# Performance work log

Hardware: AMD Instinct MI355X
Metric: run time of the kernel (lower is better)

Reference implementation:

```python
import jax, jax.numpy as jnp
import numpy as np

N, IN_DIM, OUT_DIM = 8192, 128, 128

def setup_inputs() -> dict:
    key = jax.random.key(0)
    k1, k2, k3, k4 = jax.random.split(key, 4)
    X = jax.random.normal(k1, (N, IN_DIM), dtype=jnp.float32)
    A = jax.random.uniform(k2, (N, N), dtype=jnp.float32)
    # nn.Linear(in_dim, out_dim): W [out,in], b [out]
    bound = 1.0 / np.sqrt(IN_DIM)
    W = jax.random.uniform(k3, (OUT_DIM, IN_DIM), minval=-bound, maxval=bound, dtype=jnp.float32)
    b = jax.random.uniform(k4, (OUT_DIM,), minval=-bound, maxval=bound, dtype=jnp.float32)
    return {"X": X, "A": A, "W": W, "b": b}

def reference(X, A, W, b):
    n = A.shape[0]
    A_hat = A + jnp.eye(n, dtype=A.dtype)                 # A + I
    d_inv_sqrt = A_hat.sum(axis=1) ** -0.5                # [N]
    # D^-1/2 @ A_hat @ D^-1/2 == row/col scaling (same math, no diag GEMMs)
    A_norm = d_inv_sqrt[:, None] * A_hat * d_inv_sqrt[None, :]
    H = A_norm @ X                                        # [N, in_dim]
    return H @ W.T + b                                    # [N, out_dim]
```

## Files before the change

kernel.cpp:

```cpp
#include <hip/hip_runtime.h>

#define N_NODES 8192
#define DIM 128

typedef short bf16x8 __attribute__((ext_vector_type(8)));
typedef unsigned short u16x4 __attribute__((ext_vector_type(4)));
typedef float f32x4 __attribute__((ext_vector_type(4)));

__device__ __forceinline__ unsigned short f2bf_rne(float x) {
    unsigned int u = __builtin_bit_cast(unsigned int, x);
    u += 0x7fffu + ((u >> 16) & 1u);
    return (unsigned short)(u >> 16);
}
__device__ __forceinline__ float bf2f(unsigned short h) {
    unsigned int u = ((unsigned int)h) << 16;
    return __builtin_bit_cast(float, u);
}

__global__ __launch_bounds__(256) void k_prep(const float* __restrict__ A,
                                              unsigned short* __restrict__ Abp,
                                              float* __restrict__ d) {
    __shared__ unsigned short tile[16 * 512];
    __shared__ float rs[2][8][128];
    const int t = threadIdx.x;
    const int lane = t & 63, wv = t >> 6;
    const int l15 = lane & 15, quad = lane >> 4;
    const int rb16 = blockIdx.x;
    const float* Ag0 = A + (size_t)rb16 * 16 * N_NODES;
    const int h = t >> 7;
    const int c4 = (t & 127) << 2;
    float rsum[8] = {};

    f32x4 pre[8];
#pragma unroll
    for (int i = 0; i < 8; ++i)
        pre[i] = *(const f32x4*)(Ag0 + (size_t)(h + 2 * i) * N_NODES + c4);

    for (int chunk = 0; chunk < 16; ++chunk) {
        f32x4 curv[8];
#pragma unroll
        for (int i = 0; i < 8; ++i) curv[i] = pre[i];
        if (chunk < 15) {
            const float* Ag = Ag0 + (chunk + 1) * 512;
#pragma unroll
            for (int i = 0; i < 8; ++i)
                pre[i] = *(const f32x4*)(Ag + (size_t)(h + 2 * i) * N_NODES + c4);
        }
        __syncthreads();
#pragma unroll
        for (int i = 0; i < 8; ++i) {
            int r = h + 2 * i;
            f32x4 v = curv[i];
            rsum[i] += (v[0] + v[1]) + (v[2] + v[3]);
            int byte = (r * 1024 + c4 * 2) ^ ((r & 7) << 4);
            u16x4 pk = { f2bf_rne(v[0]), f2bf_rne(v[1]), f2bf_rne(v[2]), f2bf_rne(v[3]) };
            *(u16x4*)((char*)tile + byte) = pk;
        }
        __syncthreads();
#pragma unroll
        for (int u = 0; u < 4; ++u) {
            int kk = wv * 4 + u;
            int abyte = (l15 * 1024 + (kk * 32 + quad * 8) * 2) ^ ((l15 & 7) << 4);
            bf16x8 frag = *(const bf16x8*)((const char*)tile + abyte);
            int kbg = chunk * 16 + kk;
            *(bf16x8*)(Abp + ((size_t)(rb16 * 256 + kbg) * 64 + lane) * 8) = frag;
        }
    }

#pragma unroll
    for (int i = 0; i < 8; ++i) rs[h][i][t & 127] = rsum[i];
    __syncthreads();
    if (t < 16) {
        const float* p = rs[t & 1][t >> 1];
        float s = 0.f;
        for (int j = 0; j < 128; ++j) s += p[j];
        d[rb16 * 16 + t] = rsqrtf(s + 1.0f);
    }
}

__global__ __launch_bounds__(256) void k_zgemm(const float* __restrict__ X,
                                               const float* __restrict__ W,
                                               const float* __restrict__ d,
                                               unsigned short* __restrict__ Zp) {
    __shared__ float Xs[64][129];
    __shared__ float Ws[64][129];
    int rb = blockIdx.x >> 1;
    int cb = blockIdx.x & 1;
    int t = threadIdx.x;
    const float4* Xg = (const float4*)(X + (size_t)rb * 64 * DIM);
    const float4* Wg = (const float4*)(W + (size_t)cb * 64 * DIM);
#pragma unroll
    for (int i = 0; i < 8; ++i) {
        int f = t + i * 256;
        int r = f >> 5;
        int c = (f & 31) << 2;
        float4 v = Xg[f];
        Xs[r][c] = v.x; Xs[r][c + 1] = v.y; Xs[r][c + 2] = v.z; Xs[r][c + 3] = v.w;
        float4 w = Wg[f];
        Ws[r][c] = w.x; Ws[r][c + 1] = w.y; Ws[r][c + 2] = w.z; Ws[r][c + 3] = w.w;
    }
    __syncthreads();
    int tx = t & 15, ty = t >> 4;
    float acc[4][4] = {};
    for (int k = 0; k < DIM; ++k) {
        float xr[4], wr[4];
#pragma unroll
        for (int i = 0; i < 4; ++i) xr[i] = Xs[ty * 4 + i][k];
#pragma unroll
        for (int j = 0; j < 4; ++j) wr[j] = Ws[tx * 4 + j][k];
#pragma unroll
        for (int i = 0; i < 4; ++i)
#pragma unroll
            for (int j = 0; j < 4; ++j)
                acc[i][j] += xr[i] * wr[j];
    }
#pragma unroll
    for (int i = 0; i < 4; ++i) {
        int row = rb * 64 + ty * 4 + i;
        float dv = d[row];
        int kb = row >> 5, jj = row & 7;
        int lrow = ((row >> 3) & 3) * 16;
#pragma unroll
        for (int j = 0; j < 4; ++j) {
            int col = cb * 64 + tx * 4 + j;
            int lanep = lrow + (col & 15);
            Zp[((size_t)(kb * 8 + (col >> 4)) * 64 + lanep) * 8 + jj] =
                f2bf_rne(dv * acc[i][j]);
        }
    }
}

__global__ __launch_bounds__(512, 4) void k_spmm(const unsigned short* __restrict__ Abp,
                                                 const unsigned short* __restrict__ Zp,
                                                 const float* __restrict__ d,
                                                 const float* __restrict__ bias,
                                                 float* __restrict__ out) {
    const int t = threadIdx.x;
    const int lane = t & 63, wv = t >> 6;
    const int l15 = lane & 15, quad = lane >> 4;
    const int rb16 = blockIdx.x;
    const int row0 = rb16 * 16;

    const unsigned short* Ab = Abp + ((size_t)rb16 * 256 * 64 + lane) * 8;
    const unsigned short* Zb = Zp + (size_t)lane * 8;

    f32x4 acc[8];
#pragma unroll
    for (int c = 0; c < 8; ++c) acc[c] = (f32x4){0.f, 0.f, 0.f, 0.f};

#pragma unroll 2
    for (int kb = wv * 32; kb < wv * 32 + 32; ++kb) {
        bf16x8 af = *(const bf16x8*)(Ab + (size_t)kb * 512);
        const unsigned short* zk = Zb + (size_t)kb * 4096;
#pragma unroll
        for (int c = 0; c < 8; ++c) {
            bf16x8 b = *(const bf16x8*)(zk + c * 512);
            acc[c] = __builtin_amdgcn_mfma_f32_16x16x32_bf16(af, b, acc[c], 0, 0, 0);
        }
    }

    __shared__ float red[8][64][33];
#pragma unroll
    for (int c = 0; c < 8; ++c)
#pragma unroll
        for (int r = 0; r < 4; ++r)
            red[wv][lane][c * 4 + r] = acc[c][r];
    __syncthreads();

    {
        int col = wv * 16 + l15;
        float bcol = bias[col];
#pragma unroll
        for (int r = 0; r < 4; ++r) {
            int idx = wv * 4 + r;
            float s = 0.f;
#pragma unroll
            for (int w = 0; w < 8; ++w) s += red[w][lane][idx];
            int row = row0 + quad * 4 + r;
            int kb = row >> 5, jj = row & 7;
            int lanep = ((row >> 3) & 3) * 16 + l15;
            float zid = bf2f(Zp[((size_t)(kb * 8 + wv) * 64 + lanep) * 8 + jj]);
            out[(size_t)row * DIM + col] = d[row] * (s + zid) + bcol;
        }
    }
}

extern "C" void kernel_launch(void* const* d_in, const int* in_sizes, int n_in,
                              void* d_out, int out_size, void* d_ws, size_t ws_size,
                              hipStream_t stream) {
    const float* X = (const float*)d_in[0];
    const float* A = (const float*)d_in[1];
    const float* W = (const float*)d_in[2];
    const float* b = (const float*)d_in[3];
    float* out = (float*)d_out;

    char* ws = (char*)d_ws;
    float* dinv = (float*)ws;
    unsigned short* Zp = (unsigned short*)(ws + 32768);
    unsigned short* Abp = (unsigned short*)(ws + 32768 + (2u << 20));

    k_prep<<<512, 256, 0, stream>>>(A, Abp, dinv);
    k_zgemm<<<256, 256, 0, stream>>>(X, W, dinv, Zp);
    k_spmm<<<512, 512, 0, stream>>>(Abp, Zp, dinv, b, out);
}
```

Before: 451.7 us.

## Merge two 16-row SpMM blocks into one 1024-thread block with phased reduction

The SpMM kernel now launches 256 blocks of 1024 threads, each handling two 16-row slabs: waves 0-7 take one slab and waves 8-15 the other, each split across K. The cross-wave reduction reuses one shared buffer in two phases with extra barriers, and all 16 waves join each phase's epilogue. The intent is to share Z tile reads between the two slabs through cache and halve the block count. The risks are the extra synchronization and lower scheduling flexibility from the large blocks, and the dominant A-streaming cost in k_prep is untouched.

New measurement: 456.9 us. About the same (+1.2%).

```diff
diff --git a/kernel.cpp b/kernel.cpp
--- a/kernel.cpp
+++ b/kernel.cpp
@@ -130,16 +130,19 @@
     }
 }
 
-__global__ __launch_bounds__(512, 4) void k_spmm(const unsigned short* __restrict__ Abp,
-                                                 const unsigned short* __restrict__ Zp,
-                                                 const float* __restrict__ d,
-                                                 const float* __restrict__ bias,
-                                                 float* __restrict__ out) {
+__global__ __launch_bounds__(1024) void k_spmm(const unsigned short* __restrict__ Abp,
+                                               const unsigned short* __restrict__ Zp,
+                                               const float* __restrict__ d,
+                                               const float* __restrict__ bias,
+                                               float* __restrict__ out) {
+    __shared__ float red[8][64][33];
     const int t = threadIdx.x;
-    const int lane = t & 63, wv = t >> 6;
+    const int lane = t & 63;
+    const int wv = t >> 6;
+    const int rh = wv >> 3;
+    const int kq = wv & 7;
     const int l15 = lane & 15, quad = lane >> 4;
-    const int rb16 = blockIdx.x;
-    const int row0 = rb16 * 16;
+    const int rb16 = blockIdx.x * 2 + rh;
 
     const unsigned short* Ab = Abp + ((size_t)rb16 * 256 * 64 + lane) * 8;
     const unsigned short* Zb = Zp + (size_t)lane * 8;
@@ -149,7 +152,7 @@
     for (int c = 0; c < 8; ++c) acc[c] = (f32x4){0.f, 0.f, 0.f, 0.f};
 
 #pragma unroll 2
-    for (int kb = wv * 32; kb < wv * 32 + 32; ++kb) {
+    for (int kb = kq * 32; kb < kq * 32 + 32; ++kb) {
         bf16x8 af = *(const bf16x8*)(Ab + (size_t)kb * 512);
         const unsigned short* zk = Zb + (size_t)kb * 4096;
 #pragma unroll
@@ -159,29 +162,34 @@
         }
     }
 
-    __shared__ float red[8][64][33];
-#pragma unroll
-    for (int c = 0; c < 8; ++c)
-#pragma unroll
-        for (int r = 0; r < 4; ++r)
-            red[wv][lane][c * 4 + r] = acc[c][r];
-    __syncthreads();
-
-    {
-        int col = wv * 16 + l15;
-        float bcol = bias[col];
-#pragma unroll
-        for (int r = 0; r < 4; ++r) {
-            int idx = wv * 4 + r;
-            float s = 0.f;
-#pragma unroll
-            for (int w = 0; w < 8; ++w) s += red[w][lane][idx];
-            int row = row0 + quad * 4 + r;
-            int kb = row >> 5, jj = row & 7;
-            int lanep = ((row >> 3) & 3) * 16 + l15;
-            float zid = bf2f(Zp[((size_t)(kb * 8 + wv) * 64 + lanep) * 8 + jj]);
-            out[(size_t)row * DIM + col] = d[row] * (s + zid) + bcol;
-        }
+    for (int ph = 0; ph < 2; ++ph) {
+        if (rh == ph) {
+#pragma unroll
+            for (int c = 0; c < 8; ++c)
+#pragma unroll
+                for (int r = 0; r < 4; ++r)
+                    red[kq][lane][c * 4 + r] = acc[c][r];
+        }
+        __syncthreads();
+        {
+            int c = wv & 7;
+            int rpair = wv >> 3;
+            int col = c * 16 + l15;
+            float bcol = bias[col];
+#pragma unroll
+            for (int rr = 0; rr < 2; ++rr) {
+                int r = rpair * 2 + rr;
+                float s = 0.f;
+#pragma unroll
+                for (int k8 = 0; k8 < 8; ++k8) s += red[k8][lane][c * 4 + r];
+                int row = blockIdx.x * 32 + ph * 16 + quad * 4 + r;
+                int kbr = row >> 5, jj = row & 7;
+                int lanep = ((row >> 3) & 3) * 16 + l15;
+                float zid = bf2f(Zp[((size_t)(kbr * 8 + c) * 64 + lanep) * 8 + jj]);
+                out[(size_t)row * DIM + col] = d[row] * (s + zid) + bcol;
+            }
+        }
+        __syncthreads();
     }
 }
 
@@ -201,5 +209,5 @@
 
     k_prep<<<512, 256, 0, stream>>>(A, Abp, dinv);
     k_zgemm<<<256, 256, 0, stream>>>(X, W, dinv, Zp);
-    k_spmm<<<512, 512, 0, stream>>>(Abp, Zp, dinv, b, out);
-}
+    k_spmm<<<256, 1024, 0, stream>>>(Abp, Zp, dinv, b, out);
+}
```

## Split SpMM work by output column per wave and widen prep blocks

Applied to the files above, without the earlier changes.

In k_spmm each wave now owns one 16-column slice of the output and walks the full K dimension, instead of owning a K-slice across all columns. This removes the large LDS cross-wave reduction and its barrier. Every wave now re-reads the same A fragments, eight times per block, which raises A traffic that caches must absorb, and there is less ILP per wave. k_prep moves to 512 threads per block with half the rows per thread, aiming for more memory parallelism.

New measurement: 475.4 us. 1.05x slower.

```diff
diff --git a/kernel.cpp b/kernel.cpp
--- a/kernel.cpp
+++ b/kernel.cpp
@@ -17,11 +17,11 @@
     return __builtin_bit_cast(float, u);
 }
 
-__global__ __launch_bounds__(256) void k_prep(const float* __restrict__ A,
+__global__ __launch_bounds__(512) void k_prep(const float* __restrict__ A,
                                               unsigned short* __restrict__ Abp,
                                               float* __restrict__ d) {
     __shared__ unsigned short tile[16 * 512];
-    __shared__ float rs[2][8][128];
+    __shared__ float rs[4][4][128];
     const int t = threadIdx.x;
     const int lane = t & 63, wv = t >> 6;
     const int l15 = lane & 15, quad = lane >> 4;
@@ -29,27 +29,27 @@
     const float* Ag0 = A + (size_t)rb16 * 16 * N_NODES;
     const int h = t >> 7;
     const int c4 = (t & 127) << 2;
-    float rsum[8] = {};
+    float rsum[4] = {};
 
-    f32x4 pre[8];
+    f32x4 pre[4];
 #pragma unroll
-    for (int i = 0; i < 8; ++i)
-        pre[i] = *(const f32x4*)(Ag0 + (size_t)(h + 2 * i) * N_NODES + c4);
+    for (int i = 0; i < 4; ++i)
+        pre[i] = *(const f32x4*)(Ag0 + (size_t)(h + 4 * i) * N_NODES + c4);
 
     for (int chunk = 0; chunk < 16; ++chunk) {
-        f32x4 curv[8];
+        f32x4 curv[4];
 #pragma unroll
-        for (int i = 0; i < 8; ++i) curv[i] = pre[i];
+        for (int i = 0; i < 4; ++i) curv[i] = pre[i];
         if (chunk < 15) {
             const float* Ag = Ag0 + (chunk + 1) * 512;
 #pragma unroll
-            for (int i = 0; i < 8; ++i)
-                pre[i] = *(const f32x4*)(Ag + (size_t)(h + 2 * i) * N_NODES + c4);
+            for (int i = 0; i < 4; ++i)
+                pre[i] = *(const f32x4*)(Ag + (size_t)(h + 4 * i) * N_NODES + c4);
         }
         __syncthreads();
 #pragma unroll
-        for (int i = 0; i < 8; ++i) {
-            int r = h + 2 * i;
+        for (int i = 0; i < 4; ++i) {
+            int r = h + 4 * i;
             f32x4 v = curv[i];
             rsum[i] += (v[0] + v[1]) + (v[2] + v[3]);
             int byte = (r * 1024 + c4 * 2) ^ ((r & 7) << 4);
@@ -58,8 +58,8 @@
         }
         __syncthreads();
 #pragma unroll
-        for (int u = 0; u < 4; ++u) {
-            int kk = wv * 4 + u;
+        for (int u = 0; u < 2; ++u) {
+            int kk = wv * 2 + u;
             int abyte = (l15 * 1024 + (kk * 32 + quad * 8) * 2) ^ ((l15 & 7) << 4);
             bf16x8 frag = *(const bf16x8*)((const char*)tile + abyte);
             int kbg = chunk * 16 + kk;
@@ -68,10 +68,10 @@
     }
 
 #pragma unroll
-    for (int i = 0; i < 8; ++i) rs[h][i][t & 127] = rsum[i];
+    for (int i = 0; i < 4; ++i) rs[h][i][t & 127] = rsum[i];
     __syncthreads();
     if (t < 16) {
-        const float* p = rs[t & 1][t >> 1];
+        const float* p = rs[t & 3][t >> 2];
         float s = 0.f;
         for (int j = 0; j < 128; ++j) s += p[j];
         d[rb16 * 16 + t] = rsqrtf(s + 1.0f);
@@ -130,11 +130,11 @@
     }
 }
 
-__global__ __launch_bounds__(512, 4) void k_spmm(const unsigned short* __restrict__ Abp,
-                                                 const unsigned short* __restrict__ Zp,
-                                                 const float* __restrict__ d,
-                                                 const float* __restrict__ bias,
-                                                 float* __restrict__ out) {
+__global__ __launch_bounds__(512) void k_spmm(const unsigned short* __restrict__ Abp,
+                                              const unsigned short* __restrict__ Zp,
+                                              const float* __restrict__ d,
+                                              const float* __restrict__ bias,
+                                              float* __restrict__ out) {
     const int t = threadIdx.x;
     const int lane = t & 63, wv = t >> 6;
     const int l15 = lane & 15, quad = lane >> 4;
@@ -142,46 +142,30 @@
     const int row0 = rb16 * 16;
 
     const unsigned short* Ab = Abp + ((size_t)rb16 * 256 * 64 + lane) * 8;
-    const unsigned short* Zb = Zp + (size_t)lane * 8;
+    const unsigned short* Zb = Zp + ((size_t)wv * 64 + lane) * 8;
 
-    f32x4 acc[8];
-#pragma unroll
-    for (int c = 0; c < 8; ++c) acc[c] = (f32x4){0.f, 0.f, 0.f, 0.f};
+    f32x4 acc0 = {0.f, 0.f, 0.f, 0.f}, acc1 = {0.f, 0.f, 0.f, 0.f};
 
-#pragma unroll 2
-    for (int kb = wv * 32; kb < wv * 32 + 32; ++kb) {
-        bf16x8 af = *(const bf16x8*)(Ab + (size_t)kb * 512);
-        const unsigned short* zk = Zb + (size_t)kb * 4096;
-#pragma unroll
-        for (int c = 0; c < 8; ++c) {
-            bf16x8 b = *(const bf16x8*)(zk + c * 512);
-            acc[c] = __builtin_amdgcn_mfma_f32_16x16x32_bf16(af, b, acc[c], 0, 0, 0);
-        }
+#pragma unroll 4
+    for (int kb = 0; kb < 256; kb += 2) {
+        bf16x8 af0 = *(const bf16x8*)(Ab + (size_t)kb * 512);
+        bf16x8 b0  = *(const bf16x8*)(Zb + (size_t)kb * 4096);
+        bf16x8 af1 = *(const bf16x8*)(Ab + (size_t)(kb + 1) * 512);
+        bf16x8 b1  = *(const bf16x8*)(Zb + (size_t)(kb + 1) * 4096);
+        acc0 = __builtin_amdgcn_mfma_f32_16x16x32_bf16(af0, b0, acc0, 0, 0, 0);
+        acc1 = __builtin_amdgcn_mfma_f32_16x16x32_bf16(af1, b1, acc1, 0, 0, 0);
     }
 
-    __shared__ float red[8][64][33];
+    int col = wv * 16 + l15;
+    float bcol = bias[col];
 #pragma unroll
-    for (int c = 0; c < 8; ++c)
-#pragma unroll
-        for (int r = 0; r < 4; ++r)
-            red[wv][lane][c * 4 + r] = acc[c][r];
-    __syncthreads();
-
-    {
-        int col = wv * 16 + l15;
-        float bcol = bias[col];
-#pragma unroll
-        for (int r = 0; r < 4; ++r) {
-            int idx = wv * 4 + r;
-            float s = 0.f;
-#pragma unroll
-            for (int w = 0; w < 8; ++w) s += red[w][lane][idx];
-            int row = row0 + quad * 4 + r;
-            int kb = row >> 5, jj = row & 7;
-            int lanep = ((row >> 3) & 3) * 16 + l15;
-            float zid = bf2f(Zp[((size_t)(kb * 8 + wv) * 64 + lanep) * 8 + jj]);
-            out[(size_t)row * DIM + col] = d[row] * (s + zid) + bcol;
-        }
+    for (int r = 0; r < 4; ++r) {
+        int row = row0 + quad * 4 + r;
+        float s = acc0[r] + acc1[r];
+        int kbr = row >> 5, jj = row & 7;
+        int lanep = ((row >> 3) & 3) * 16 + l15;
+        float zid = bf2f(Zp[((size_t)(kbr * 8 + wv) * 64 + lanep) * 8 + jj]);
+        out[(size_t)row * DIM + col] = d[row] * (s + zid) + bcol;
     }
 }
 
@@ -199,7 +183,7 @@
     unsigned short* Zp = (unsigned short*)(ws + 32768);
     unsigned short* Abp = (unsigned short*)(ws + 32768 + (2u << 20));
 
-    k_prep<<<512, 256, 0, stream>>>(A, Abp, dinv);
+    k_prep<<<512, 512, 0, stream>>>(A, Abp, dinv);
     k_zgemm<<<256, 256, 0, stream>>>(X, W, dinv, Zp);
     k_spmm<<<512, 512, 0, stream>>>(Abp, Zp, dinv, b, out);
 }
```
